# Optimization experiments

Measured on AMD Instinct MI355X. Metric: run time of the kernel, lower is better.

Reference implementation:

```python
import jax, jax.numpy as jnp
import numpy as np

MAX_ITERS = 50
EPS_NORM = 1e-8
EPS_SEP = -1e-6


def setup_inputs() -> dict:
    key = jax.random.key(0)
    k1, k2 = jax.random.split(key)
    pointcloud = jax.random.normal(k1, (200000, 3), dtype=jnp.float32)
    targets = jax.random.normal(k2, (256, 3), dtype=jnp.float32)
    return {"pointcloud": pointcloud, "targets": targets}


def reference(pointcloud, targets):
    # pointcloud: [N, d], targets: [M, d]
    N = pointcloud.shape[0]
    M = targets.shape[0]
    p2 = jnp.sum(pointcloud * pointcloud, axis=1)  # [N]
    t2 = jnp.sum(targets * targets, axis=1)        # [M]

    def step(mask, _):
        # squared euclidean distances [M, N] (argmin identical to cdist argmin)
        d2 = t2[:, None] + p2[None, :] - 2.0 * (targets @ pointcloud.T)
        d2 = jnp.where(mask, d2, jnp.inf)
        closest_idx = jnp.argmin(d2, axis=1)           # [M]
        closest_points = pointcloud[closest_idx]       # [M, d]
        a = closest_points - targets
        a = a / (jnp.linalg.norm(a, axis=1, keepdims=True) + EPS_NORM)
        b = jnp.sum(a * closest_points, axis=1)        # [M]
        dot = a @ pointcloud.T - b[:, None]            # [M, N]
        separated = dot >= EPS_SEP
        mask = mask & ~separated
        return mask, (a, b)

    mask0 = jnp.ones((M, N), dtype=bool)
    _, (a_stack, b_stack) = jax.lax.scan(step, mask0, None, length=MAX_ITERS)
    return a_stack, b_stack  # [MAX_ITERS, M, d], [MAX_ITERS, M]
```

## Files before the change

kernel.cpp:

```cpp
#include <hip/hip_runtime.h>
#include <stdint.h>
#include <math.h>

#pragma clang fp contract(off)

#define BLOCK 1024
#define NW (BLOCK / 64)
#define PT 8
#define PB 4
#define MAX_ITERS 50
#define SOLO_CAP 2048
#define EPS_NORM 1e-8f
#define EPS_SEP (-1e-6f)

__global__ void pack_points(const float* __restrict__ pc,
                            float4* __restrict__ pk,
                            float* __restrict__ sx, float* __restrict__ sy,
                            float* __restrict__ sz, int N, int mode) {
    const int i = blockIdx.x * blockDim.x + threadIdx.x;
    if (i < N) {
        const float x = pc[3*i+0], y = pc[3*i+1], z = pc[3*i+2];
        float4 v; v.x = x; v.y = y; v.z = z;
        v.w = x*x + y*y + z*z;
        pk[i] = v;
        if (mode >= 2) { sx[i] = x; sy[i] = y; sz[i] = z; }
    }
}

template <int MODE>
__global__ __launch_bounds__(BLOCK) void convex_plane_kernel(
    const float* __restrict__ pc, const float4* __restrict__ pk,
    const float* __restrict__ sx, const float* __restrict__ sy,
    const float* __restrict__ sz, const float* __restrict__ tg,
    float* __restrict__ out, int N, int M, int CAP, int stepsA)
{
    extern __shared__ uint32_t smem[];
    const int tid  = threadIdx.x;
    const int lane = tid & 63;
    const int wv   = tid >> 6;
    const int m    = blockIdx.x;

    const int maskW = stepsA * (PT * BLOCK / 32);
    uint32_t* mask  = smem;
    int*      list  = (int*)(smem + maskW);
    float*    red_d = (float*)(list + CAP);
    int*      red_i = (int*)(red_d + NW);
    int*      cw    = red_i + NW;
    int*      bcast = cw + NW;
    int*      cnt   = bcast + 2;

    const float tx = tg[3*m+0], ty = tg[3*m+1], tz = tg[3*m+2];
    const float t2 = tx*tx + ty*ty + tz*tz;

    float* out_a = out;
    float* out_b = out + (size_t)MAX_ITERS * (size_t)M * 3;

    auto ldp = [&](int ip, float& x, float& y, float& z, float& w) {
        if constexpr (MODE >= 1) {
            const float4 v = pk[ip];
            x = v.x; y = v.y; z = v.z; w = v.w;
        } else {
            const float* p = pc + 3 * (size_t)ip;
            x = p[0]; y = p[1]; z = p[2];
            w = x*x + y*y + z*z;
        }
    };

    auto finish = [&](float dmin, int imin, int mycnt, bool cntFromCursor) -> int2 {
        #pragma unroll
        for (int off = 32; off > 0; off >>= 1) {
            float od = __shfl_down(dmin, off, 64);
            int   oi = __shfl_down(imin, off, 64);
            int   oc = __shfl_down(mycnt, off, 64);
            if (od < dmin || (od == dmin && oi < imin)) { dmin = od; imin = oi; }
            mycnt += oc;
        }
        if (lane == 0) { red_d[wv] = dmin; red_i[wv] = imin; cw[wv] = mycnt; }
        __syncthreads();
        if (wv == 0) {
            float bd = (lane < NW) ? red_d[lane] : INFINITY;
            int   bi = (lane < NW) ? red_i[lane] : 0;
            int   c  = (lane < NW) ? cw[lane]    : 0;
            #pragma unroll
            for (int off = 8; off > 0; off >>= 1) {
                float od = __shfl_down(bd, off, 64);
                int   oi = __shfl_down(bi, off, 64);
                int   oc = __shfl_down(c,  off, 64);
                if (od < bd || (od == bd && oi < bi)) { bd = od; bi = oi; }
                c += oc;
            }
            if (lane == 0) { bcast[0] = bi; bcast[1] = cntFromCursor ? cnt[0] : c; }
        }
        __syncthreads();
        int2 r; r.x = bcast[0]; r.y = bcast[1];
        return r;
    };

    auto scanA = [&](int mode, bool build,
                     float ax, float ay, float az, float b) -> int2 {
        if (tid == 0) cnt[0] = 0;
        __syncthreads();
        float dmin = INFINITY;
        int   imin = 0;
        int   mycnt = 0;
        for (int s = 0; s < stepsA; ++s) {
            const int ib    = s * PT * BLOCK + tid;
            const int wbase = s * (PT * BLOCK / 32);
            uint32_t live = 0;
            if (mode == 2) {
                #pragma unroll
                for (int j = 0; j < PT; ++j) {
                    uint32_t w = mask[wbase + j * (BLOCK / 32) + (tid >> 5)];
                    live |= ((w >> (tid & 31)) & 1u) << j;
                }
            } else {
                #pragma unroll
                for (int j = 0; j < PT; ++j)
                    if (ib + j * BLOCK < N) live |= (1u << j);
            }
            float px[PT], py[PT], pz[PT], pw[PT];
            if constexpr (MODE == 2) {
                #pragma unroll
                for (int j = 0; j < PT; ++j) {
                    int ip = ib + j * BLOCK;
                    ip = ip < N ? ip : N - 1;
                    px[j] = sx[ip]; py[j] = sy[ip]; pz[j] = sz[ip];
                }
                #pragma unroll
                for (int j = 0; j < PT; ++j)
                    pw[j] = px[j]*px[j] + py[j]*py[j] + pz[j]*pz[j];
            } else {
                #pragma unroll
                for (int j = 0; j < PT; ++j) {
                    int ip = ib + j * BLOCK;
                    ip = ip < N ? ip : N - 1;
                    ldp(ip, px[j], py[j], pz[j], pw[j]);
                }
            }
            uint32_t keepm = 0;
            #pragma unroll
            for (int j = 0; j < PT; ++j) {
                if ((live >> j) & 1u) {
                    bool keep;
                    if (mode == 0) keep = true;
                    else {
                        float dt = ax*px[j] + ay*py[j] + az*pz[j] - b;
                        keep = (dt < EPS_SEP);
                    }
                    if (keep) {
                        keepm |= (1u << j);
                        float tp = tx*px[j] + ty*py[j] + tz*pz[j];
                        float d2 = t2 + pw[j] - 2.0f*tp;
                        const int i = ib + j * BLOCK;
                        if (d2 < dmin || (d2 == dmin && i < imin)) {
                            dmin = d2; imin = i;
                        }
                    }
                }
            }
            if (mode != 0) {
                #pragma unroll
                for (int j = 0; j < PT; ++j) {
                    unsigned long long bal = __ballot(((keepm >> j) & 1u) != 0u);
                    const int widx = wbase + j * (BLOCK / 32) + (wv << 1);
                    if (lane == 0)       mask[widx]     = (uint32_t)bal;
                    else if (lane == 32) mask[widx + 1] = (uint32_t)(bal >> 32);
                }
            }
            mycnt += (int)__popc(keepm);
            if (build) {
                int c = (int)__popc(keepm);
                int incl = c;
                #pragma unroll
                for (int off = 1; off < 64; off <<= 1) {
                    int o = __shfl_up(incl, off, 64);
                    if (lane >= off) incl += o;
                }
                const int excl = incl - c;
                const int tot  = __shfl(incl, 63, 64);
                int wb = 0;
                if (lane == 0) wb = atomicAdd(cnt, tot);
                wb = __shfl(wb, 0, 64);
                int pos = wb + excl;
                #pragma unroll
                for (int j = 0; j < PT; ++j) {
                    if ((keepm >> j) & 1u) {
                        if (pos < CAP) list[pos] = ib + j * BLOCK;
                        ++pos;
                    }
                }
            }
        }
        return finish(dmin, imin, mycnt, false);
    };

    auto scanB = [&](int count, float ax, float ay, float az, float b) -> int2 {
        if (tid == 0) cnt[0] = 0;
        __syncthreads();
        float dmin = INFINITY;
        int   imin = 0;
        const int per = BLOCK * PB;
        const int bsteps = (count + per - 1) / per;
        for (int s = 0; s < bsteps; ++s) {
            int jv[PB]; float d2v[PB];
            uint32_t keepm = 0;
            #pragma unroll
            for (int q = 0; q < PB; ++q) {
                const int e = s * per + q * BLOCK + tid;
                if (e < count) {
                    const int j = list[e];
                    jv[q] = j;
                    float px, py, pz, p2;
                    ldp(j, px, py, pz, p2);
                    float dt = ax*px + ay*py + az*pz - b;
                    if (dt < EPS_SEP) {
                        keepm |= (1u << q);
                        float tp = tx*px + ty*py + tz*pz;
                        d2v[q] = t2 + p2 - 2.0f*tp;
                    }
                }
            }
            __syncthreads();
            int c = (int)__popc(keepm);
            int incl = c;
            #pragma unroll
            for (int off = 1; off < 64; off <<= 1) {
                int o = __shfl_up(incl, off, 64);
                if (lane >= off) incl += o;
            }
            const int excl = incl - c;
            const int tot  = __shfl(incl, 63, 64);
            int wb = 0;
            if (lane == 0) wb = atomicAdd(cnt, tot);
            wb = __shfl(wb, 0, 64);
            int pos = wb + excl;
            #pragma unroll
            for (int q = 0; q < PB; ++q) {
                if ((keepm >> q) & 1u) {
                    list[pos] = jv[q];
                    if (d2v[q] < dmin || (d2v[q] == dmin && jv[q] < imin)) {
                        dmin = d2v[q]; imin = jv[q];
                    }
                    ++pos;
                }
            }
        }
        __syncthreads();
        return finish(dmin, imin, 0, true);
    };

    bool comp = false;
    int2 rc = scanA(0, false, 0.f, 0.f, 0.f, 0.f);
    int idx = rc.x, count = rc.y;

    for (int k = 0; k < MAX_ITERS; ++k) {
        if (comp && count <= SOLO_CAP) {
            float* lx = (float*)(list + SOLO_CAP);
            float* ly = lx + SOLO_CAP;
            float* lz = ly + SOLO_CAP;
            for (int e = tid; e < count; e += BLOCK) {
                float x, y, z, w;
                ldp(list[e], x, y, z, w);
                lx[e] = x; ly[e] = y; lz[e] = z;
            }
            __syncthreads();
            if (wv != 0) return;
            for (; k < MAX_ITERS; ++k) {
                float cx, cy, cz, cw4;
                ldp(idx, cx, cy, cz, cw4);
                const float vx = cx - tx, vy = cy - ty, vz = cz - tz;
                const float nrm = sqrtf(vx*vx + vy*vy + vz*vz);
                const float den = nrm + EPS_NORM;
                const float ax = vx / den, ay = vy / den, az = vz / den;
                const float b  = ax*cx + ay*cy + az*cz;
                if (count == 0) {
                    for (int q = lane; q < MAX_ITERS - k; q += 64) {
                        const int kk = k + q;
                        const size_t oa = ((size_t)kk * M + m) * 3;
                        out_a[oa+0] = ax; out_a[oa+1] = ay; out_a[oa+2] = az;
                        out_b[(size_t)kk * M + m] = b;
                    }
                    return;
                }
                if (lane == 0) {
                    const size_t oa = ((size_t)k * M + m) * 3;
                    out_a[oa+0] = ax; out_a[oa+1] = ay; out_a[oa+2] = az;
                    out_b[(size_t)k * M + m] = b;
                }
                if (k + 1 < MAX_ITERS) {
                    float dmin = INFINITY; int imin = 0; int wcur = 0;
                    for (int e0 = 0; e0 < count; e0 += 64) {
                        const int e = e0 + lane;
                        bool keep = false; int j = 0;
                        float d2v = 0.f, px = 0.f, py = 0.f, pz = 0.f;
                        if (e < count) {
                            j = list[e];
                            px = lx[e]; py = ly[e]; pz = lz[e];
                            float dt = ax*px + ay*py + az*pz - b;
                            if (dt < EPS_SEP) {
                                keep = true;
                                float p2 = px*px + py*py + pz*pz;
                                float tp = tx*px + ty*py + tz*pz;
                                d2v = t2 + p2 - 2.0f*tp;
                            }
                        }
                        unsigned long long bal = __ballot(keep);
                        int pos = wcur + (int)__popcll(bal & ((1ull << lane) - 1ull));
                        if (keep) {
                            list[pos] = j;
                            lx[pos] = px; ly[pos] = py; lz[pos] = pz;
                            if (d2v < dmin || (d2v == dmin && j < imin)) {
                                dmin = d2v; imin = j;
                            }
                        }
                        wcur += (int)__popcll(bal);
                    }
                    #pragma unroll
                    for (int off = 32; off > 0; off >>= 1) {
                        float od = __shfl_down(dmin, off, 64);
                        int   oi = __shfl_down(imin, off, 64);
                        if (od < dmin || (od == dmin && oi < imin)) { dmin = od; imin = oi; }
                    }
                    idx = __shfl(imin, 0, 64);
                    count = wcur;
                }
            }
            return;
        }

        float cx, cy, cz, cw4;
        ldp(idx, cx, cy, cz, cw4);
        const float vx = cx - tx, vy = cy - ty, vz = cz - tz;
        const float nrm = sqrtf(vx*vx + vy*vy + vz*vz);
        const float den = nrm + EPS_NORM;
        const float ax = vx / den, ay = vy / den, az = vz / den;
        const float b  = ax*cx + ay*cy + az*cz;

        if (count == 0) {
            for (int q = tid; q < MAX_ITERS - k; q += BLOCK) {
                const int kk = k + q;
                const size_t oa = ((size_t)kk * M + m) * 3;
                out_a[oa+0] = ax; out_a[oa+1] = ay; out_a[oa+2] = az;
                out_b[(size_t)kk * M + m] = b;
            }
            return;
        }
        if (tid == 0) {
            const size_t oa = ((size_t)k * M + m) * 3;
            out_a[oa+0] = ax; out_a[oa+1] = ay; out_a[oa+2] = az;
            out_b[(size_t)k * M + m] = b;
        }
        if (k + 1 < MAX_ITERS) {
            if (comp) {
                rc = scanB(count, ax, ay, az, b);
            } else {
                const bool build = (count <= 2 * CAP);
                rc = scanA(k == 0 ? 1 : 2, build, ax, ay, az, b);
                if (build && rc.y <= CAP) comp = true;
            }
            idx = rc.x; count = rc.y;
        }
    }
}

extern "C" void kernel_launch(void* const* d_in, const int* in_sizes, int n_in,
                              void* d_out, int out_size, void* d_ws, size_t ws_size,
                              hipStream_t stream) {
    const float* pc = (const float*)d_in[0];
    const float* tg = (const float*)d_in[1];
    float* out = (float*)d_out;
    const int N = in_sizes[0] / 3;
    const int M = in_sizes[1] / 3;
    const int stepsA = (N + BLOCK * PT - 1) / (BLOCK * PT);
    const size_t maskB  = (size_t)stepsA * (PT * BLOCK / 32) * sizeof(uint32_t);
    const size_t fixedB = NW * (2 * sizeof(int) + sizeof(float)) + 3 * sizeof(int);
    const size_t need16 = (size_t)N * sizeof(float4);
    const size_t need28 = need16 + 3 * (size_t)N * sizeof(float);

    int wsmode = 0;
    if (d_ws && ws_size >= need28) wsmode = 2;
    else if (d_ws && ws_size >= need16) wsmode = 1;

    float4* pk = (float4*)d_ws;
    float*  sxp = (float*)((char*)d_ws + need16);
    float*  syp = sxp + N;
    float*  szp = syp + N;

    int CAP = 32768;
    size_t smem = maskB + (size_t)CAP * sizeof(int) + fixedB;
    const void* fn = (wsmode == 2) ? (const void*)convex_plane_kernel<2>
                   : (wsmode == 1) ? (const void*)convex_plane_kernel<1>
                                   : (const void*)convex_plane_kernel<0>;
    if (hipFuncSetAttribute(fn, hipFuncAttributeMaxDynamicSharedMemorySize,
                            (int)smem) != hipSuccess) {
        CAP = 8192;
        smem = maskB + (size_t)CAP * sizeof(int) + fixedB;
    }
    if (wsmode >= 1) {
        pack_points<<<(N + 255) / 256, 256, 0, stream>>>(pc, pk, sxp, syp, szp,
                                                         N, wsmode);
    }
    if (wsmode == 2) {
        convex_plane_kernel<2><<<M, BLOCK, smem, stream>>>(
            pc, pk, sxp, syp, szp, tg, out, N, M, CAP, stepsA);
    } else if (wsmode == 1) {
        convex_plane_kernel<1><<<M, BLOCK, smem, stream>>>(
            pc, pk, nullptr, nullptr, nullptr, tg, out, N, M, CAP, stepsA);
    } else {
        convex_plane_kernel<0><<<M, BLOCK, smem, stream>>>(
            pc, nullptr, nullptr, nullptr, nullptr, tg, out, N, M, CAP, stepsA);
    }
}
```

Baseline: 598.0 us.

## Compact surviving points into per-target global float4 lists

Result: faster. 551.3 us (-7.8%).

```diff
diff --git a/kernel.cpp b/kernel.cpp
--- a/kernel.cpp
+++ b/kernel.cpp
@@ -14,25 +14,21 @@
 #define EPS_SEP (-1e-6f)
 
 __global__ void pack_points(const float* __restrict__ pc,
-                            float4* __restrict__ pk,
-                            float* __restrict__ sx, float* __restrict__ sy,
-                            float* __restrict__ sz, int N, int mode) {
+                            float4* __restrict__ pk, int N) {
     const int i = blockIdx.x * blockDim.x + threadIdx.x;
     if (i < N) {
         const float x = pc[3*i+0], y = pc[3*i+1], z = pc[3*i+2];
         float4 v; v.x = x; v.y = y; v.z = z;
         v.w = x*x + y*y + z*z;
         pk[i] = v;
-        if (mode >= 2) { sx[i] = x; sy[i] = y; sz[i] = z; }
     }
 }
 
 template <int MODE>
 __global__ __launch_bounds__(BLOCK) void convex_plane_kernel(
     const float* __restrict__ pc, const float4* __restrict__ pk,
-    const float* __restrict__ sx, const float* __restrict__ sy,
-    const float* __restrict__ sz, const float* __restrict__ tg,
-    float* __restrict__ out, int N, int M, int CAP, int stepsA)
+    float4* __restrict__ glist, const float* __restrict__ tg,
+    float* __restrict__ out, int N, int M, int CAP, int CAPG, int stepsA)
 {
     extern __shared__ uint32_t smem[];
     const int tid  = threadIdx.x;
@@ -49,6 +45,8 @@
     int*      bcast = cw + NW;
     int*      cnt   = bcast + 2;
 
+    float4* gl = (MODE == 3) ? glist + (size_t)m * (size_t)CAPG : nullptr;
+
     const float tx = tg[3*m+0], ty = tg[3*m+1], tz = tg[3*m+2];
     const float t2 = tx*tx + ty*ty + tz*tz;
 
@@ -96,7 +94,7 @@
         return r;
     };
 
-    auto scanA = [&](int mode, bool build,
+    auto scanA = [&](int mode, bool buildL, bool buildG,
                      float ax, float ay, float az, float b) -> int2 {
         if (tid == 0) cnt[0] = 0;
         __syncthreads();
@@ -119,23 +117,11 @@
                     if (ib + j * BLOCK < N) live |= (1u << j);
             }
             float px[PT], py[PT], pz[PT], pw[PT];
-            if constexpr (MODE == 2) {
-                #pragma unroll
-                for (int j = 0; j < PT; ++j) {
-                    int ip = ib + j * BLOCK;
-                    ip = ip < N ? ip : N - 1;
-                    px[j] = sx[ip]; py[j] = sy[ip]; pz[j] = sz[ip];
-                }
-                #pragma unroll
-                for (int j = 0; j < PT; ++j)
-                    pw[j] = px[j]*px[j] + py[j]*py[j] + pz[j]*pz[j];
-            } else {
-                #pragma unroll
-                for (int j = 0; j < PT; ++j) {
-                    int ip = ib + j * BLOCK;
-                    ip = ip < N ? ip : N - 1;
-                    ldp(ip, px[j], py[j], pz[j], pw[j]);
-                }
+            #pragma unroll
+            for (int j = 0; j < PT; ++j) {
+                int ip = ib + j * BLOCK;
+                ip = ip < N ? ip : N - 1;
+                ldp(ip, px[j], py[j], pz[j], pw[j]);
             }
             uint32_t keepm = 0;
             #pragma unroll
@@ -168,7 +154,7 @@
                 }
             }
             mycnt += (int)__popc(keepm);
-            if (build) {
+            if (buildL || buildG) {
                 int c = (int)__popc(keepm);
                 int incl = c;
                 #pragma unroll
@@ -185,13 +171,81 @@
                 #pragma unroll
                 for (int j = 0; j < PT; ++j) {
                     if ((keepm >> j) & 1u) {
-                        if (pos < CAP) list[pos] = ib + j * BLOCK;
+                        const int i = ib + j * BLOCK;
+                        if (buildL && pos < CAP) list[pos] = i;
+                        if constexpr (MODE == 3) {
+                            if (buildG && pos < CAPG) {
+                                float4 v; v.x = px[j]; v.y = py[j];
+                                v.z = pz[j]; v.w = __int_as_float(i);
+                                gl[pos] = v;
+                            }
+                        }
                         ++pos;
                     }
                 }
             }
         }
         return finish(dmin, imin, mycnt, false);
+    };
+
+    auto scanG = [&](int count, float ax, float ay, float az, float b) -> int2 {
+        if (tid == 0) cnt[0] = 0;
+        __syncthreads();
+        float dmin = INFINITY;
+        int   imin = 0;
+        const int per = BLOCK * PB;
+        const int bsteps = (count + per - 1) / per;
+        for (int s = 0; s < bsteps; ++s) {
+            float4 v[PB]; float d2v[PB]; int iv[PB];
+            uint32_t keepm = 0;
+            #pragma unroll
+            for (int q = 0; q < PB; ++q) {
+                int e = s * per + q * BLOCK + tid;
+                e = e < count ? e : count - 1;
+                v[q] = gl[e];
+            }
+            #pragma unroll
+            for (int q = 0; q < PB; ++q) {
+                const int e = s * per + q * BLOCK + tid;
+                if (e < count) {
+                    const float x = v[q].x, y = v[q].y, z = v[q].z;
+                    iv[q] = __float_as_int(v[q].w);
+                    float dt = ax*x + ay*y + az*z - b;
+                    if (dt < EPS_SEP) {
+                        keepm |= (1u << q);
+                        float p2 = x*x + y*y + z*z;
+                        float tp = tx*x + ty*y + tz*z;
+                        d2v[q] = t2 + p2 - 2.0f*tp;
+                    }
+                }
+            }
+            __syncthreads();
+            int c = (int)__popc(keepm);
+            int incl = c;
+            #pragma unroll
+            for (int off = 1; off < 64; off <<= 1) {
+                int o = __shfl_up(incl, off, 64);
+                if (lane >= off) incl += o;
+            }
+            const int excl = incl - c;
+            const int tot  = __shfl(incl, 63, 64);
+            int wb = 0;
+            if (lane == 0) wb = atomicAdd(cnt, tot);
+            wb = __shfl(wb, 0, 64);
+            int pos = wb + excl;
+            #pragma unroll
+            for (int q = 0; q < PB; ++q) {
+                if ((keepm >> q) & 1u) {
+                    gl[pos] = v[q];
+                    if (d2v[q] < dmin || (d2v[q] == dmin && iv[q] < imin)) {
+                        dmin = d2v[q]; imin = iv[q];
+                    }
+                    ++pos;
+                }
+            }
+        }
+        __syncthreads();
+        return finish(dmin, imin, 0, true);
     };
 
     auto scanB = [&](int count, float ax, float ay, float az, float b) -> int2 {
@@ -249,19 +303,29 @@
         return finish(dmin, imin, 0, true);
     };
 
-    bool comp = false;
-    int2 rc = scanA(0, false, 0.f, 0.f, 0.f, 0.f);
+    bool comp = false, compG = false;
+    int2 rc = scanA(0, false, false, 0.f, 0.f, 0.f, 0.f);
     int idx = rc.x, count = rc.y;
 
     for (int k = 0; k < MAX_ITERS; ++k) {
-        if (comp && count <= SOLO_CAP) {
+        if ((comp || compG) && count <= SOLO_CAP) {
             float* lx = (float*)(list + SOLO_CAP);
             float* ly = lx + SOLO_CAP;
             float* lz = ly + SOLO_CAP;
-            for (int e = tid; e < count; e += BLOCK) {
-                float x, y, z, w;
-                ldp(list[e], x, y, z, w);
-                lx[e] = x; ly[e] = y; lz[e] = z;
+            if (compG) {
+                if constexpr (MODE == 3) {
+                    for (int e = tid; e < count; e += BLOCK) {
+                        const float4 v = gl[e];
+                        lx[e] = v.x; ly[e] = v.y; lz[e] = v.z;
+                        list[e] = __float_as_int(v.w);
+                    }
+                }
+            } else {
+                for (int e = tid; e < count; e += BLOCK) {
+                    float x, y, z, w;
+                    ldp(list[e], x, y, z, w);
+                    lx[e] = x; ly[e] = y; lz[e] = z;
+                }
             }
             __syncthreads();
             if (wv != 0) return;
@@ -351,12 +415,16 @@
             out_b[(size_t)k * M + m] = b;
         }
         if (k + 1 < MAX_ITERS) {
-            if (comp) {
+            if (compG) {
+                rc = scanG(count, ax, ay, az, b);
+            } else if (comp) {
                 rc = scanB(count, ax, ay, az, b);
             } else {
-                const bool build = (count <= 2 * CAP);
-                rc = scanA(k == 0 ? 1 : 2, build, ax, ay, az, b);
-                if (build && rc.y <= CAP) comp = true;
+                const bool bG = (MODE == 3) && CAPG > 0 && count <= 2 * CAPG;
+                const bool bL = count <= 2 * CAP;
+                rc = scanA(k == 0 ? 1 : 2, bL, bG, ax, ay, az, b);
+                if (bG && rc.y <= CAPG) compG = true;
+                else if (bL && rc.y <= CAP) comp = true;
             }
             idx = rc.x; count = rc.y;
         }
@@ -374,21 +442,23 @@
     const int stepsA = (N + BLOCK * PT - 1) / (BLOCK * PT);
     const size_t maskB  = (size_t)stepsA * (PT * BLOCK / 32) * sizeof(uint32_t);
     const size_t fixedB = NW * (2 * sizeof(int) + sizeof(float)) + 3 * sizeof(int);
-    const size_t need16 = (size_t)N * sizeof(float4);
-    const size_t need28 = need16 + 3 * (size_t)N * sizeof(float);
+    const size_t pkB    = (size_t)N * sizeof(float4);
 
     int wsmode = 0;
-    if (d_ws && ws_size >= need28) wsmode = 2;
-    else if (d_ws && ws_size >= need16) wsmode = 1;
-
+    int CAPG = 0;
+    if (d_ws && ws_size >= pkB) {
+        wsmode = 1;
+        const size_t rem = ws_size - pkB;
+        size_t cg = rem / ((size_t)M * sizeof(float4));
+        if (cg > 131072) cg = 131072;
+        if (cg >= 8192) { CAPG = (int)cg; wsmode = 3; }
+    }
     float4* pk = (float4*)d_ws;
-    float*  sxp = (float*)((char*)d_ws + need16);
-    float*  syp = sxp + N;
-    float*  szp = syp + N;
+    float4* glp = (float4*)((char*)d_ws + pkB);
 
     int CAP = 32768;
     size_t smem = maskB + (size_t)CAP * sizeof(int) + fixedB;
-    const void* fn = (wsmode == 2) ? (const void*)convex_plane_kernel<2>
+    const void* fn = (wsmode == 3) ? (const void*)convex_plane_kernel<3>
                    : (wsmode == 1) ? (const void*)convex_plane_kernel<1>
                                    : (const void*)convex_plane_kernel<0>;
     if (hipFuncSetAttribute(fn, hipFuncAttributeMaxDynamicSharedMemorySize,
@@ -397,17 +467,16 @@
         smem = maskB + (size_t)CAP * sizeof(int) + fixedB;
     }
     if (wsmode >= 1) {
-        pack_points<<<(N + 255) / 256, 256, 0, stream>>>(pc, pk, sxp, syp, szp,
-                                                         N, wsmode);
-    }
-    if (wsmode == 2) {
-        convex_plane_kernel<2><<<M, BLOCK, smem, stream>>>(
-            pc, pk, sxp, syp, szp, tg, out, N, M, CAP, stepsA);
+        pack_points<<<(N + 255) / 256, 256, 0, stream>>>(pc, pk, N);
+    }
+    if (wsmode == 3) {
+        convex_plane_kernel<3><<<M, BLOCK, smem, stream>>>(
+            pc, pk, glp, tg, out, N, M, CAP, CAPG, stepsA);
     } else if (wsmode == 1) {
         convex_plane_kernel<1><<<M, BLOCK, smem, stream>>>(
-            pc, pk, nullptr, nullptr, nullptr, tg, out, N, M, CAP, stepsA);
+            pc, pk, nullptr, tg, out, N, M, CAP, 0, stepsA);
     } else {
         convex_plane_kernel<0><<<M, BLOCK, smem, stream>>>(
-            pc, nullptr, nullptr, nullptr, nullptr, tg, out, N, M, CAP, stepsA);
+            pc, nullptr, nullptr, tg, out, N, M, CAP, 0, stepsA);
     }
 }
```
